# Kernel tuning notes

Hardware: AMD Instinct MI355X
Metric: run time of the kernel (lower is better)

## Reference

```python
import jax, jax.numpy as jnp
import numpy as np

B, N, D = 8, 4096, 2048
DL = 64
NCLS = 2


def setup_inputs() -> dict:
    key = jax.random.key(0)
    k_x, k_tn, k_v, k_w, k_fw, k_fb = jax.random.split(key, 6)
    x = jax.random.normal(k_x, (B, N, D), dtype=jnp.float32)
    # valid patch counts in [1, N] so no bag is fully masked
    true_num = jax.random.randint(k_tn, (B,), 1, N + 1, dtype=jnp.int32)
    std1 = 1.0 / np.sqrt(DL * D)
    V = jax.random.uniform(k_v, (D, DL), minval=-std1, maxval=std1, dtype=jnp.float32)
    std2 = 1.0 / np.sqrt(DL)
    W = jax.random.uniform(k_w, (DL, 1), minval=-std2, maxval=std2, dtype=jnp.float32)
    lim = 1.0 / np.sqrt(D)  # nn.Linear default init
    fc_w = jax.random.uniform(k_fw, (NCLS, D), minval=-lim, maxval=lim, dtype=jnp.float32)
    fc_b = jax.random.uniform(k_fb, (NCLS,), minval=-lim, maxval=lim, dtype=jnp.float32)
    return {"x": x, "true_num": true_num, "V": V, "W": W, "fc_w": fc_w, "fc_b": fc_b}


def reference(x, true_num, V, W, fc_w, fc_b):
    # MILAtten: attention scores over N patches
    x_ = jnp.tanh(jnp.einsum("bnd,dl->bnl", x, V))            # B x N x dl
    dis = jnp.einsum("bnl,lo->bn", x_, W) / np.sqrt(DL)        # B x N
    mask = jnp.arange(x.shape[1])[None, :] < true_num[:, None]  # B x N valid mask
    dis = jnp.where(mask, dis, jnp.float32(-1e20))
    soft_assign = jax.nn.softmax(dis, axis=1)                  # B x N
    feat_fusion = jnp.einsum("bn,bnd->bd", soft_assign, x)     # B x D
    # eval mode: dropout is identity
    logits = feat_fusion @ fc_w.T + fc_b                       # B x class_num
    cls_probs = jax.nn.softmax(logits, axis=1)
    return (cls_probs, soft_assign)
```

## Files before the change

kernel.cpp:

```cpp
#include <hip/hip_runtime.h>
#include <math.h>

#define BB 8
#define NN 4096
#define DD 2048

typedef __attribute__((ext_vector_type(8))) short bf16x8;
typedef __attribute__((ext_vector_type(4))) float f32x4;

__device__ __forceinline__ short f2bf(float f) {
    unsigned int u = __float_as_uint(f);
    unsigned int r = (u + 0x7fffu + ((u >> 16) & 1u)) >> 16;
    return (short)r;
}
__device__ __forceinline__ float bf2f(short s) {
    return __uint_as_float(((unsigned int)(unsigned short)s) << 16);
}

__global__ __launch_bounds__(256) void k_pack_v(const float* __restrict__ V,
                                                short* __restrict__ Vp) {
    int e = blockIdx.x * 256 + threadIdx.x;
    int lane = e & 63, kc = (e >> 6) & 63, w = e >> 12;
    int q = lane >> 4, mm = lane & 15;
    int kb = kc * 32 + q * 8, l = w * 16 + mm;
    bf16x8 o;
    #pragma unroll
    for (int j = 0; j < 8; j++) o[j] = f2bf(V[(size_t)(kb + j) * 64 + l]);
    *(bf16x8*)(Vp + (size_t)e * 8) = o;
}

__global__ __launch_bounds__(256, 2) void k_fused(
        const float* __restrict__ x, const int* __restrict__ tn_p,
        const short* __restrict__ Vp, const float* __restrict__ W,
        const float* __restrict__ fc_w,
        float* __restrict__ dis, float* __restrict__ mblk,
        float* __restrict__ lblk, float* __restrict__ qblk,
        float* __restrict__ dpart, float* __restrict__ erow_g) {
    __shared__ short Xs[16 * 2048];

    const int tid = threadIdx.x;
    const int blk = blockIdx.x;
    const int b  = blk >> 8;
    const int n0 = (blk & 255) << 4;
    const int tn = tn_p[b];
    if (n0 >= tn) return;

    const int lane = tid & 63, w = tid >> 6;
    const int mm = lane & 15, q = lane >> 4;

    const f32x4* xsrc = (const f32x4*)(x + ((size_t)(b * NN + n0)) * DD);
    #pragma unroll 8
    for (int i = 0; i < 32; i++) {
        int e = tid + (i << 8);
        int row = e >> 9, f4 = e & 511;
        f32x4 v = __builtin_nontemporal_load(&xsrc[(size_t)row * 512 + f4]);
        int c = f4 >> 1, h = f4 & 1;
        int sc = c ^ (row & 7);
        short4 s;
        s.x = f2bf(v.x); s.y = f2bf(v.y); s.z = f2bf(v.z); s.w = f2bf(v.w);
        *(short4*)&Xs[row * 2048 + sc * 8 + h * 4] = s;
    }

    const bf16x8* vpv = (const bf16x8*)Vp + ((size_t)w << 12) + lane;
    bf16x8 bvr[4];
    #pragma unroll
    for (int j = 0; j < 4; j++) bvr[j] = vpv[j << 6];
    const float wl = W[w * 16 + mm];

    __syncthreads();

    const int arow = mm * 2048;
    const int msw = mm & 7;
    f32x4 acc = {0.f, 0.f, 0.f, 0.f};
    #pragma unroll
    for (int kc = 0; kc < 64; kc += 4) {
        bf16x8 cur0 = bvr[0], cur1 = bvr[1], cur2 = bvr[2], cur3 = bvr[3];
        if (kc + 4 < 64) {
            #pragma unroll
            for (int j = 0; j < 4; j++) bvr[j] = vpv[(kc + 4 + j) << 6];
        }
        bf16x8 a0 = *(const bf16x8*)&Xs[arow + ((((kc + 0) * 4 + q) ^ msw) << 3)];
        acc = __builtin_amdgcn_mfma_f32_16x16x32_bf16(a0, cur0, acc, 0, 0, 0);
        bf16x8 a1 = *(const bf16x8*)&Xs[arow + ((((kc + 1) * 4 + q) ^ msw) << 3)];
        acc = __builtin_amdgcn_mfma_f32_16x16x32_bf16(a1, cur1, acc, 0, 0, 0);
        bf16x8 a2 = *(const bf16x8*)&Xs[arow + ((((kc + 2) * 4 + q) ^ msw) << 3)];
        acc = __builtin_amdgcn_mfma_f32_16x16x32_bf16(a2, cur2, acc, 0, 0, 0);
        bf16x8 a3 = *(const bf16x8*)&Xs[arow + ((((kc + 3) * 4 + q) ^ msw) << 3)];
        acc = __builtin_amdgcn_mfma_f32_16x16x32_bf16(a3, cur3, acc, 0, 0, 0);
    }

    const float4* w0p = (const float4*)fc_w + tid * 2;
    const float4* w1p = (const float4*)(fc_w + DD) + tid * 2;
    float4 wa = w0p[0], wb = w0p[1], wc = w1p[0], wd = w1p[1];

    float* dpb = dpart + blk * 64;
    #pragma unroll
    for (int r = 0; r < 4; r++) {
        float p = tanhf(acc[r]) * wl;
        p += __shfl_xor(p, 1, 64);
        p += __shfl_xor(p, 2, 64);
        p += __shfl_xor(p, 4, 64);
        p += __shfl_xor(p, 8, 64);
        if (mm == 0) dpb[w * 16 + q * 4 + r] = p;
    }
    __syncthreads();

    if (w == 0) {
        float d = (dpb[mm] + dpb[16 + mm] + dpb[32 + mm] + dpb[48 + mm]) * 0.125f;
        int n = n0 + mm;
        if (n >= tn) d = -1e20f;
        if (lane < 16) dis[b * NN + n] = d;
        float mx = d;
        mx = fmaxf(mx, __shfl_xor(mx, 1, 64));
        mx = fmaxf(mx, __shfl_xor(mx, 2, 64));
        mx = fmaxf(mx, __shfl_xor(mx, 4, 64));
        mx = fmaxf(mx, __shfl_xor(mx, 8, 64));
        float e = expf(d - mx);
        float ls = e;
        ls += __shfl_xor(ls, 1, 64);
        ls += __shfl_xor(ls, 2, 64);
        ls += __shfl_xor(ls, 4, 64);
        ls += __shfl_xor(ls, 8, 64);
        if (lane < 16) erow_g[blk * 16 + lane] = e;
        if (lane == 0) { mblk[blk] = mx; lblk[blk] = ls; }
    }
    __syncthreads();

    float er[16];
    const float* eg = erow_g + blk * 16;
    #pragma unroll
    for (int r = 0; r < 16; r++) er[r] = eg[r];

    float facc[8];
    #pragma unroll
    for (int u = 0; u < 8; u++) facc[u] = 0.f;
    #pragma unroll
    for (int r = 0; r < 16; r++) {
        bf16x8 sv = *(const bf16x8*)&Xs[r * 2048 + ((tid ^ (r & 7)) << 3)];
        float e = er[r];
        #pragma unroll
        for (int u = 0; u < 8; u++) facc[u] = fmaf(e, bf2f(sv[u]), facc[u]);
    }
    float q0 = facc[0] * wa.x + facc[1] * wa.y + facc[2] * wa.z + facc[3] * wa.w +
               facc[4] * wb.x + facc[5] * wb.y + facc[6] * wb.z + facc[7] * wb.w;
    float q1 = facc[0] * wc.x + facc[1] * wc.y + facc[2] * wc.z + facc[3] * wc.w +
               facc[4] * wd.x + facc[5] * wd.y + facc[6] * wd.z + facc[7] * wd.w;
    #pragma unroll
    for (int o = 32; o >= 1; o >>= 1) {
        q0 += __shfl_xor(q0, o, 64);
        q1 += __shfl_xor(q1, o, 64);
    }
    if (lane == 0) {
        qblk[blk * 8 + w * 2 + 0] = q0;
        qblk[blk * 8 + w * 2 + 1] = q1;
    }
}

__global__ __launch_bounds__(256) void k_final(
        const float* __restrict__ dis, const int* __restrict__ tn_p,
        const float* __restrict__ mblk, const float* __restrict__ lblk,
        const float* __restrict__ qblk, const float* __restrict__ fc_b,
        float* __restrict__ soft, float* __restrict__ cls) {
    __shared__ float red[4];
    __shared__ float r3[3][4];
    __shared__ float bc;
    const int b = blockIdx.x >> 2, s = blockIdx.x & 3, t = threadIdx.x;
    const int tn = tn_p[b];
    const int nvb = (tn + 15) >> 4;

    float mt = (t < nvb) ? mblk[b * 256 + t] : -3.4e38f;
    float mx = mt;
    #pragma unroll
    for (int o = 32; o >= 1; o >>= 1) mx = fmaxf(mx, __shfl_xor(mx, o, 64));
    if ((t & 63) == 0) red[t >> 6] = mx;
    __syncthreads();
    if (t == 0) bc = fmaxf(fmaxf(red[0], red[1]), fmaxf(red[2], red[3]));
    __syncthreads();
    const float M = bc;

    float sc = (t < nvb) ? expf(mt - M) : 0.f;
    float ls = (t < nvb) ? sc * lblk[b * 256 + t] : 0.f;
    float l0 = 0.f, l1 = 0.f;
    if (t < nvb) {
        const float* qp = qblk + (size_t)(b * 256 + t) * 8;
        l0 = sc * (qp[0] + qp[2] + qp[4] + qp[6]);
        l1 = sc * (qp[1] + qp[3] + qp[5] + qp[7]);
    }
    #pragma unroll
    for (int o = 32; o >= 1; o >>= 1) {
        ls += __shfl_xor(ls, o, 64);
        l0 += __shfl_xor(l0, o, 64);
        l1 += __shfl_xor(l1, o, 64);
    }
    if ((t & 63) == 0) {
        r3[0][t >> 6] = ls; r3[1][t >> 6] = l0; r3[2][t >> 6] = l1;
    }
    __syncthreads();
    if (t == 0) {
        float L  = r3[0][0] + r3[0][1] + r3[0][2] + r3[0][3];
        bc = 1.f / L;
        if (s == 0) {
            float Q0 = r3[1][0] + r3[1][1] + r3[1][2] + r3[1][3];
            float Q1 = r3[2][0] + r3[2][1] + r3[2][2] + r3[2][3];
            float L0 = Q0 / L + fc_b[0];
            float L1 = Q1 / L + fc_b[1];
            float mm2 = fmaxf(L0, L1);
            float e0 = expf(L0 - mm2), e1 = expf(L1 - mm2);
            float inv = 1.f / (e0 + e1);
            cls[b * 2 + 0] = e0 * inv;
            cls[b * 2 + 1] = e1 * inv;
        }
    }
    __syncthreads();
    const float iL = bc;

    const int i = s * 256 + t;
    const int n = i * 4;
    float4 dv = ((const float4*)(dis + (size_t)b * NN))[i];
    float4 o;
    o.x = (n + 0 < tn) ? expf(dv.x - M) * iL : 0.f;
    o.y = (n + 1 < tn) ? expf(dv.y - M) * iL : 0.f;
    o.z = (n + 2 < tn) ? expf(dv.z - M) * iL : 0.f;
    o.w = (n + 3 < tn) ? expf(dv.w - M) * iL : 0.f;
    ((float4*)(soft + (size_t)b * NN))[i] = o;
}

extern "C" void kernel_launch(void* const* d_in, const int* in_sizes, int n_in,
                              void* d_out, int out_size, void* d_ws, size_t ws_size,
                              hipStream_t stream) {
    (void)in_sizes; (void)n_in; (void)out_size; (void)ws_size;
    const float* x        = (const float*)d_in[0];
    const int*   true_num = (const int*)d_in[1];
    const float* V        = (const float*)d_in[2];
    const float* W        = (const float*)d_in[3];
    const float* fc_w     = (const float*)d_in[4];
    const float* fc_b     = (const float*)d_in[5];

    float* out  = (float*)d_out;
    float* cls  = out;
    float* soft = out + BB * 2;

    float* dis   = (float*)d_ws;
    float* mblk  = dis + (size_t)BB * NN;
    float* lblk  = mblk + 2048;
    float* qblk  = lblk + 2048;
    float* dpart = qblk + (size_t)2048 * 8;
    float* erow  = dpart + (size_t)2048 * 64;
    short* Vp    = (short*)(erow + (size_t)2048 * 16);

    k_pack_v<<<64, 256, 0, stream>>>(V, Vp);
    k_fused<<<2048, 256, 0, stream>>>(x, true_num, Vp, W, fc_w,
                                      dis, mblk, lblk, qblk, dpart, erow);
    k_final<<<32, 256, 0, stream>>>(dis, true_num, mblk, lblk, qblk, fc_b,
                                    soft, cls);
}
```

Before: 340.7 us.

## Stream x rows via global_load_lds double buffer and keep partials in LDS

Replaces the register-staged fp32 load of the 16x2048 x tile with asynchronous global_load_lds into a two-row fp32 LDS ring buffer. Each row is converted to bf16 into the swizzled tile while later rows are still in flight, using explicit vmcnt waits. The per-block dot partials and exp weights now live in shared memory instead of global workspace, which removes global round-trips. The cost is an extra 16KB of LDS per block, which may lower occupancy, and the hand-set vmcnt counts must match the number of outstanding loads exactly.

```diff
diff --git a/kernel.cpp b/kernel.cpp
--- a/kernel.cpp
+++ b/kernel.cpp
@@ -7,6 +7,8 @@
 
 typedef __attribute__((ext_vector_type(8))) short bf16x8;
 typedef __attribute__((ext_vector_type(4))) float f32x4;
+typedef const __attribute__((address_space(1))) unsigned gu32;
+typedef __attribute__((address_space(3))) unsigned lu32;
 
 __device__ __forceinline__ short f2bf(float f) {
     unsigned int u = __float_as_uint(f);
@@ -34,9 +36,9 @@
         const short* __restrict__ Vp, const float* __restrict__ W,
         const float* __restrict__ fc_w,
         float* __restrict__ dis, float* __restrict__ mblk,
-        float* __restrict__ lblk, float* __restrict__ qblk,
-        float* __restrict__ dpart, float* __restrict__ erow_g) {
-    __shared__ short Xs[16 * 2048];
+        float* __restrict__ lblk, float* __restrict__ qblk) {
+    __shared__ __align__(16) short Xs[16 * 2048];
+    __shared__ __align__(16) float Fbuf[2 * 2048];
 
     const int tid = threadIdx.x;
     const int blk = blockIdx.x;
@@ -48,24 +50,42 @@
     const int lane = tid & 63, w = tid >> 6;
     const int mm = lane & 15, q = lane >> 4;
 
-    const f32x4* xsrc = (const f32x4*)(x + ((size_t)(b * NN + n0)) * DD);
-    #pragma unroll 8
-    for (int i = 0; i < 32; i++) {
-        int e = tid + (i << 8);
-        int row = e >> 9, f4 = e & 511;
-        f32x4 v = __builtin_nontemporal_load(&xsrc[(size_t)row * 512 + f4]);
-        int c = f4 >> 1, h = f4 & 1;
-        int sc = c ^ (row & 7);
-        short4 s;
-        s.x = f2bf(v.x); s.y = f2bf(v.y); s.z = f2bf(v.z); s.w = f2bf(v.w);
-        *(short4*)&Xs[row * 2048 + sc * 8 + h * 4] = s;
-    }
-
+    const float* xrow = x + ((size_t)(b * NN + n0)) * DD;
+
+#define ISSUE(r) do { \
+    const float* s0_ = xrow + (size_t)(r) * DD + (w << 9) + (lane << 2); \
+    float* d0_ = Fbuf + (((r) & 1) << 11) + (w << 9); \
+    __builtin_amdgcn_global_load_lds((gu32*)(s0_),       (lu32*)(d0_),       16, 0, 0); \
+    __builtin_amdgcn_global_load_lds((gu32*)(s0_ + 256), (lu32*)(d0_ + 256), 16, 0, 0); \
+} while (0)
+
+#define CONV(r, VM) do { \
+    asm volatile("s_waitcnt vmcnt(" #VM ")" ::: "memory"); \
+    const float* f_ = Fbuf + (((r) & 1) << 11) + (w << 9) + (lane << 3); \
+    f32x4 lo = *(const f32x4*)f_; \
+    f32x4 hi = *(const f32x4*)(f_ + 4); \
+    bf16x8 o_; \
+    o_[0] = f2bf(lo.x); o_[1] = f2bf(lo.y); o_[2] = f2bf(lo.z); o_[3] = f2bf(lo.w); \
+    o_[4] = f2bf(hi.x); o_[5] = f2bf(hi.y); o_[6] = f2bf(hi.z); o_[7] = f2bf(hi.w); \
+    int c_ = (w << 6) + lane; \
+    *(bf16x8*)&Xs[(r) * 2048 + ((c_ ^ ((r) & 7)) << 3)] = o_; \
+    if ((r) + 2 < 16) ISSUE((r) + 2); \
+} while (0)
+
+    ISSUE(0); ISSUE(1);
+    asm volatile("" ::: "memory");
     const bf16x8* vpv = (const bf16x8*)Vp + ((size_t)w << 12) + lane;
     bf16x8 bvr[4];
     #pragma unroll
     for (int j = 0; j < 4; j++) bvr[j] = vpv[j << 6];
     const float wl = W[w * 16 + mm];
+    CONV(0, 7);  CONV(1, 7);
+    CONV(2, 2);  CONV(3, 2);  CONV(4, 2);  CONV(5, 2);
+    CONV(6, 2);  CONV(7, 2);  CONV(8, 2);  CONV(9, 2);
+    CONV(10, 2); CONV(11, 2); CONV(12, 2); CONV(13, 2);
+    CONV(14, 2); CONV(15, 0);
+#undef CONV
+#undef ISSUE
 
     __syncthreads();
 
@@ -93,7 +113,9 @@
     const float4* w1p = (const float4*)(fc_w + DD) + tid * 2;
     float4 wa = w0p[0], wb = w0p[1], wc = w1p[0], wd = w1p[1];
 
-    float* dpb = dpart + blk * 64;
+    float* dp  = Fbuf;
+    float* ers = Fbuf + 64;
+
     #pragma unroll
     for (int r = 0; r < 4; r++) {
         float p = tanhf(acc[r]) * wl;
@@ -101,12 +123,12 @@
         p += __shfl_xor(p, 2, 64);
         p += __shfl_xor(p, 4, 64);
         p += __shfl_xor(p, 8, 64);
-        if (mm == 0) dpb[w * 16 + q * 4 + r] = p;
+        if (mm == 0) dp[w * 16 + q * 4 + r] = p;
     }
     __syncthreads();
 
     if (w == 0) {
-        float d = (dpb[mm] + dpb[16 + mm] + dpb[32 + mm] + dpb[48 + mm]) * 0.125f;
+        float d = (dp[mm] + dp[16 + mm] + dp[32 + mm] + dp[48 + mm]) * 0.125f;
         int n = n0 + mm;
         if (n >= tn) d = -1e20f;
         if (lane < 16) dis[b * NN + n] = d;
@@ -121,15 +143,10 @@
         ls += __shfl_xor(ls, 2, 64);
         ls += __shfl_xor(ls, 4, 64);
         ls += __shfl_xor(ls, 8, 64);
-        if (lane < 16) erow_g[blk * 16 + lane] = e;
+        if (lane < 16) ers[lane] = e;
         if (lane == 0) { mblk[blk] = mx; lblk[blk] = ls; }
     }
     __syncthreads();
-
-    float er[16];
-    const float* eg = erow_g + blk * 16;
-    #pragma unroll
-    for (int r = 0; r < 16; r++) er[r] = eg[r];
 
     float facc[8];
     #pragma unroll
@@ -137,7 +154,7 @@
     #pragma unroll
     for (int r = 0; r < 16; r++) {
         bf16x8 sv = *(const bf16x8*)&Xs[r * 2048 + ((tid ^ (r & 7)) << 3)];
-        float e = er[r];
+        float e = ers[r];
         #pragma unroll
         for (int u = 0; u < 8; u++) facc[u] = fmaf(e, bf2f(sv[u]), facc[u]);
     }
@@ -244,13 +261,11 @@
     float* mblk  = dis + (size_t)BB * NN;
     float* lblk  = mblk + 2048;
     float* qblk  = lblk + 2048;
-    float* dpart = qblk + (size_t)2048 * 8;
-    float* erow  = dpart + (size_t)2048 * 64;
-    short* Vp    = (short*)(erow + (size_t)2048 * 16);
+    short* Vp    = (short*)(qblk + (size_t)2048 * 8);
 
     k_pack_v<<<64, 256, 0, stream>>>(V, Vp);
     k_fused<<<2048, 256, 0, stream>>>(x, true_num, Vp, W, fc_w,
-                                      dis, mblk, lblk, qblk, dpart, erow);
+                                      dis, mblk, lblk, qblk);
     k_final<<<32, 256, 0, stream>>>(dis, true_num, mblk, lblk, qblk, fc_b,
                                     soft, cls);
 }
```

After: 351.5 us. 1.03x slower.

## Double block threads with split-K MFMA and shared-memory intra-block reductions

Applied to the files above, without the earlier changes.

Raises the fused kernel from 256 to 512 threads per block. The 64-chunk K loop is split across two wave groups whose partial accumulators are combined through shared memory. The per-block score partials and exp weights now live in shared memory instead of global scratch, and the weighted-sum stage uses 4 columns per thread, so the q partials per block double to 16 entries, which the final kernel now sums. The aim is more waves in flight to hide x load latency, and removing global round-trips, at the cost of an extra barrier and reduction step.

```diff
diff --git a/kernel.cpp b/kernel.cpp
--- a/kernel.cpp
+++ b/kernel.cpp
@@ -29,14 +29,16 @@
     *(bf16x8*)(Vp + (size_t)e * 8) = o;
 }
 
-__global__ __launch_bounds__(256, 2) void k_fused(
+__global__ __launch_bounds__(512, 4) void k_fused(
         const float* __restrict__ x, const int* __restrict__ tn_p,
         const short* __restrict__ Vp, const float* __restrict__ W,
         const float* __restrict__ fc_w,
         float* __restrict__ dis, float* __restrict__ mblk,
-        float* __restrict__ lblk, float* __restrict__ qblk,
-        float* __restrict__ dpart, float* __restrict__ erow_g) {
-    __shared__ short Xs[16 * 2048];
+        float* __restrict__ lblk, float* __restrict__ qblk) {
+    __shared__ __align__(16) short Xs[16 * 2048];
+    __shared__ __align__(16) float comb[4 * 64 * 4];
+    __shared__ float dp[64];
+    __shared__ float ers[16];
 
     const int tid = threadIdx.x;
     const int blk = blockIdx.x;
@@ -46,26 +48,26 @@
     if (n0 >= tn) return;
 
     const int lane = tid & 63, w = tid >> 6;
+    const int wc = w & 3, wk = w >> 2;
     const int mm = lane & 15, q = lane >> 4;
 
     const f32x4* xsrc = (const f32x4*)(x + ((size_t)(b * NN + n0)) * DD);
+    const int cch = tid >> 1, hh = tid & 1;
     #pragma unroll 8
-    for (int i = 0; i < 32; i++) {
-        int e = tid + (i << 8);
-        int row = e >> 9, f4 = e & 511;
-        f32x4 v = __builtin_nontemporal_load(&xsrc[(size_t)row * 512 + f4]);
-        int c = f4 >> 1, h = f4 & 1;
-        int sc = c ^ (row & 7);
+    for (int r = 0; r < 16; r++) {
+        f32x4 v = __builtin_nontemporal_load(&xsrc[(size_t)r * 512 + tid]);
+        int sc = cch ^ (r & 7);
         short4 s;
         s.x = f2bf(v.x); s.y = f2bf(v.y); s.z = f2bf(v.z); s.w = f2bf(v.w);
-        *(short4*)&Xs[row * 2048 + sc * 8 + h * 4] = s;
-    }
-
-    const bf16x8* vpv = (const bf16x8*)Vp + ((size_t)w << 12) + lane;
+        *(short4*)&Xs[r * 2048 + sc * 8 + hh * 4] = s;
+    }
+
+    const bf16x8* vpv = (const bf16x8*)Vp + ((size_t)wc << 12) + lane;
+    const int kbase = wk << 5;
     bf16x8 bvr[4];
     #pragma unroll
-    for (int j = 0; j < 4; j++) bvr[j] = vpv[j << 6];
-    const float wl = W[w * 16 + mm];
+    for (int j = 0; j < 4; j++) bvr[j] = vpv[(kbase + j) << 6];
+    const float wl = W[wc * 16 + mm];
 
     __syncthreads();
 
@@ -73,40 +75,45 @@
     const int msw = mm & 7;
     f32x4 acc = {0.f, 0.f, 0.f, 0.f};
     #pragma unroll
-    for (int kc = 0; kc < 64; kc += 4) {
+    for (int kc = 0; kc < 32; kc += 4) {
         bf16x8 cur0 = bvr[0], cur1 = bvr[1], cur2 = bvr[2], cur3 = bvr[3];
-        if (kc + 4 < 64) {
+        if (kc + 4 < 32) {
             #pragma unroll
-            for (int j = 0; j < 4; j++) bvr[j] = vpv[(kc + 4 + j) << 6];
+            for (int j = 0; j < 4; j++) bvr[j] = vpv[(kbase + kc + 4 + j) << 6];
         }
-        bf16x8 a0 = *(const bf16x8*)&Xs[arow + ((((kc + 0) * 4 + q) ^ msw) << 3)];
+        bf16x8 a0 = *(const bf16x8*)&Xs[arow + ((((kbase + kc + 0) * 4 + q) ^ msw) << 3)];
         acc = __builtin_amdgcn_mfma_f32_16x16x32_bf16(a0, cur0, acc, 0, 0, 0);
-        bf16x8 a1 = *(const bf16x8*)&Xs[arow + ((((kc + 1) * 4 + q) ^ msw) << 3)];
+        bf16x8 a1 = *(const bf16x8*)&Xs[arow + ((((kbase + kc + 1) * 4 + q) ^ msw) << 3)];
         acc = __builtin_amdgcn_mfma_f32_16x16x32_bf16(a1, cur1, acc, 0, 0, 0);
-        bf16x8 a2 = *(const bf16x8*)&Xs[arow + ((((kc + 2) * 4 + q) ^ msw) << 3)];
+        bf16x8 a2 = *(const bf16x8*)&Xs[arow + ((((kbase + kc + 2) * 4 + q) ^ msw) << 3)];
         acc = __builtin_amdgcn_mfma_f32_16x16x32_bf16(a2, cur2, acc, 0, 0, 0);
-        bf16x8 a3 = *(const bf16x8*)&Xs[arow + ((((kc + 3) * 4 + q) ^ msw) << 3)];
+        bf16x8 a3 = *(const bf16x8*)&Xs[arow + ((((kbase + kc + 3) * 4 + q) ^ msw) << 3)];
         acc = __builtin_amdgcn_mfma_f32_16x16x32_bf16(a3, cur3, acc, 0, 0, 0);
     }
 
-    const float4* w0p = (const float4*)fc_w + tid * 2;
-    const float4* w1p = (const float4*)(fc_w + DD) + tid * 2;
-    float4 wa = w0p[0], wb = w0p[1], wc = w1p[0], wd = w1p[1];
-
-    float* dpb = dpart + blk * 64;
-    #pragma unroll
-    for (int r = 0; r < 4; r++) {
-        float p = tanhf(acc[r]) * wl;
-        p += __shfl_xor(p, 1, 64);
-        p += __shfl_xor(p, 2, 64);
-        p += __shfl_xor(p, 4, 64);
-        p += __shfl_xor(p, 8, 64);
-        if (mm == 0) dpb[w * 16 + q * 4 + r] = p;
+    const float4 wa = ((const float4*)fc_w)[tid];
+    const float4 wb = ((const float4*)(fc_w + DD))[tid];
+
+    if (wk == 1) *(f32x4*)&comb[(wc * 64 + lane) * 4] = acc;
+    __syncthreads();
+
+    if (wk == 0) {
+        f32x4 o = *(const f32x4*)&comb[(wc * 64 + lane) * 4];
+        acc += o;
+        #pragma unroll
+        for (int r = 0; r < 4; r++) {
+            float p = tanhf(acc[r]) * wl;
+            p += __shfl_xor(p, 1, 64);
+            p += __shfl_xor(p, 2, 64);
+            p += __shfl_xor(p, 4, 64);
+            p += __shfl_xor(p, 8, 64);
+            if (mm == 0) dp[wc * 16 + q * 4 + r] = p;
+        }
     }
     __syncthreads();
 
     if (w == 0) {
-        float d = (dpb[mm] + dpb[16 + mm] + dpb[32 + mm] + dpb[48 + mm]) * 0.125f;
+        float d = (dp[mm] + dp[16 + mm] + dp[32 + mm] + dp[48 + mm]) * 0.125f;
         int n = n0 + mm;
         if (n >= tn) d = -1e20f;
         if (lane < 16) dis[b * NN + n] = d;
@@ -121,38 +128,31 @@
         ls += __shfl_xor(ls, 2, 64);
         ls += __shfl_xor(ls, 4, 64);
         ls += __shfl_xor(ls, 8, 64);
-        if (lane < 16) erow_g[blk * 16 + lane] = e;
+        if (lane < 16) ers[lane] = e;
         if (lane == 0) { mblk[blk] = mx; lblk[blk] = ls; }
     }
     __syncthreads();
 
-    float er[16];
-    const float* eg = erow_g + blk * 16;
-    #pragma unroll
-    for (int r = 0; r < 16; r++) er[r] = eg[r];
-
-    float facc[8];
-    #pragma unroll
-    for (int u = 0; u < 8; u++) facc[u] = 0.f;
+    float facc[4] = {0.f, 0.f, 0.f, 0.f};
     #pragma unroll
     for (int r = 0; r < 16; r++) {
-        bf16x8 sv = *(const bf16x8*)&Xs[r * 2048 + ((tid ^ (r & 7)) << 3)];
-        float e = er[r];
-        #pragma unroll
-        for (int u = 0; u < 8; u++) facc[u] = fmaf(e, bf2f(sv[u]), facc[u]);
-    }
-    float q0 = facc[0] * wa.x + facc[1] * wa.y + facc[2] * wa.z + facc[3] * wa.w +
-               facc[4] * wb.x + facc[5] * wb.y + facc[6] * wb.z + facc[7] * wb.w;
-    float q1 = facc[0] * wc.x + facc[1] * wc.y + facc[2] * wc.z + facc[3] * wc.w +
-               facc[4] * wd.x + facc[5] * wd.y + facc[6] * wd.z + facc[7] * wd.w;
+        short4 sv = *(const short4*)&Xs[r * 2048 + ((cch ^ (r & 7)) << 3) + hh * 4];
+        float e = ers[r];
+        facc[0] = fmaf(e, bf2f(sv.x), facc[0]);
+        facc[1] = fmaf(e, bf2f(sv.y), facc[1]);
+        facc[2] = fmaf(e, bf2f(sv.z), facc[2]);
+        facc[3] = fmaf(e, bf2f(sv.w), facc[3]);
+    }
+    float q0 = facc[0] * wa.x + facc[1] * wa.y + facc[2] * wa.z + facc[3] * wa.w;
+    float q1 = facc[0] * wb.x + facc[1] * wb.y + facc[2] * wb.z + facc[3] * wb.w;
     #pragma unroll
     for (int o = 32; o >= 1; o >>= 1) {
         q0 += __shfl_xor(q0, o, 64);
         q1 += __shfl_xor(q1, o, 64);
     }
     if (lane == 0) {
-        qblk[blk * 8 + w * 2 + 0] = q0;
-        qblk[blk * 8 + w * 2 + 1] = q1;
+        qblk[blk * 16 + w * 2 + 0] = q0;
+        qblk[blk * 16 + w * 2 + 1] = q1;
     }
 }
 
@@ -182,9 +182,9 @@
     float ls = (t < nvb) ? sc * lblk[b * 256 + t] : 0.f;
     float l0 = 0.f, l1 = 0.f;
     if (t < nvb) {
-        const float* qp = qblk + (size_t)(b * 256 + t) * 8;
-        l0 = sc * (qp[0] + qp[2] + qp[4] + qp[6]);
-        l1 = sc * (qp[1] + qp[3] + qp[5] + qp[7]);
+        const float* qp = qblk + (size_t)(b * 256 + t) * 16;
+        l0 = sc * (qp[0] + qp[2] + qp[4] + qp[6] + qp[8] + qp[10] + qp[12] + qp[14]);
+        l1 = sc * (qp[1] + qp[3] + qp[5] + qp[7] + qp[9] + qp[11] + qp[13] + qp[15]);
     }
     #pragma unroll
     for (int o = 32; o >= 1; o >>= 1) {
@@ -244,13 +244,11 @@
     float* mblk  = dis + (size_t)BB * NN;
     float* lblk  = mblk + 2048;
     float* qblk  = lblk + 2048;
-    float* dpart = qblk + (size_t)2048 * 8;
-    float* erow  = dpart + (size_t)2048 * 64;
-    short* Vp    = (short*)(erow + (size_t)2048 * 16);
+    short* Vp    = (short*)(qblk + (size_t)2048 * 16);
 
     k_pack_v<<<64, 256, 0, stream>>>(V, Vp);
-    k_fused<<<2048, 256, 0, stream>>>(x, true_num, Vp, W, fc_w,
-                                      dis, mblk, lblk, qblk, dpart, erow);
+    k_fused<<<2048, 512, 0, stream>>>(x, true_num, Vp, W, fc_w,
+                                      dis, mblk, lblk, qblk);
     k_final<<<32, 256, 0, stream>>>(dis, true_num, mblk, lblk, qblk, fc_b,
                                     soft, cls);
 }
```

New measurement: 336.5 us. No clear change (-1.2%).
